# Kernel optimization log

Hardware: AMD Instinct MI355X
Metric: run time of the kernel (lower is better)

Reference implementation:

```python
import jax, jax.numpy as jnp
import numpy as np

HID = 6

def setup_inputs() -> dict:
    key = jax.random.key(0)
    k1, k2, k3, k4 = jax.random.split(key, 4)
    B, IN, OUT = 4194304, 20, 6
    x = jax.random.normal(k1, (B, IN), dtype=jnp.float32)
    # nn.Linear weights: shape [out_features, in_features], bias=False
    W1 = jax.random.normal(k2, (HID, IN), dtype=jnp.float32) / np.sqrt(IN)
    W2 = jax.random.normal(k3, (HID, HID), dtype=jnp.float32) / np.sqrt(HID)
    W5 = jax.random.normal(k4, (OUT, HID), dtype=jnp.float32) / np.sqrt(HID)
    return {"x": x, "W1": W1, "W2": W2, "W5": W5}

def reference(x, W1, W2, W5):
    # x = sigmoid(linear1(x)); x = sigmoid(linear2(x)); x = linear5(x)
    h = jax.nn.sigmoid(x @ W1.T)       # [B, 6]
    h = jax.nn.sigmoid(h @ W2.T)       # [B, 6]
    return h @ W5.T                    # [B, out]
```

## Files before the change

kernel.cpp:

```cpp
#include <hip/hip_runtime.h>

#define NIN  20
#define NHID 6
#define NOUT 6
#define RPB  256
#define PAD  21

__device__ __forceinline__ float fsig(float t) {
    return __builtin_amdgcn_rcpf(1.0f + __expf(-t));
}

__global__ __launch_bounds__(256, 4)
void mlp_fused(const float* __restrict__ x,
               const float* __restrict__ W1,
               const float* __restrict__ W2,
               const float* __restrict__ W5,
               float* __restrict__ out,
               int nrows)
{
    __shared__ float sx[RPB * PAD];

    const int t = threadIdx.x;
    const long long blk_row0 = (long long)blockIdx.x * RPB;
    const int rows_here = min(RPB, nrows - (int)min((long long)nrows, blk_row0));

    const float4* __restrict__ xp4 = (const float4*)(x + blk_row0 * NIN);
    const int n4 = rows_here * 5;
#pragma unroll
    for (int k = 0; k < 5; ++k) {
        const int i = t + RPB * k;
        if (i < n4) {
            float4 v = xp4[i];
            const int r = i / 5;
            const int c = 4 * (i % 5);
            float* d = &sx[r * PAD + c];
            d[0] = v.x; d[1] = v.y; d[2] = v.z; d[3] = v.w;
        }
    }
    __syncthreads();

    if (t >= rows_here) return;

    float xr[NIN];
#pragma unroll
    for (int k = 0; k < NIN; ++k) xr[k] = sx[t * PAD + k];

    float h[NHID];
#pragma unroll
    for (int j = 0; j < NHID; ++j) {
        float a = 0.0f;
#pragma unroll
        for (int k = 0; k < NIN; ++k) a = fmaf(xr[k], W1[j * NIN + k], a);
        h[j] = fsig(a);
    }

    float g[NHID];
#pragma unroll
    for (int j = 0; j < NHID; ++j) {
        float a = 0.0f;
#pragma unroll
        for (int k = 0; k < NHID; ++k) a = fmaf(h[k], W2[j * NHID + k], a);
        g[j] = fsig(a);
    }

    float o[NOUT];
#pragma unroll
    for (int j = 0; j < NOUT; ++j) {
        float a = 0.0f;
#pragma unroll
        for (int k = 0; k < NHID; ++k) a = fmaf(g[k], W5[j * NHID + k], a);
        o[j] = a;
    }

    float2* __restrict__ op = (float2*)(out + (blk_row0 + t) * NOUT);
    op[0] = make_float2(o[0], o[1]);
    op[1] = make_float2(o[2], o[3]);
    op[2] = make_float2(o[4], o[5]);
}

extern "C" void kernel_launch(void* const* d_in, const int* in_sizes, int n_in,
                              void* d_out, int out_size, void* d_ws, size_t ws_size,
                              hipStream_t stream) {
    const float* x  = (const float*)d_in[0];
    const float* W1 = (const float*)d_in[1];
    const float* W2 = (const float*)d_in[2];
    const float* W5 = (const float*)d_in[3];
    float* out = (float*)d_out;

    const int nrows = in_sizes[0] / NIN;
    const int grid  = (nrows + RPB - 1) / RPB;
    mlp_fused<<<grid, RPB, 0, stream>>>(x, W1, W2, W5, out, nrows);
}
```

Before: 469.4 us.

## Process four row chunks per block with register prefetch of next chunk

Each block now handles four 256-row chunks. While the current chunk is computed from shared memory, the next chunk's input is loaded into registers, so global loads overlap with compute and the grid shrinks fourfold. This adds an extra barrier per chunk and more register pressure, and with fewer blocks there is less parallelism available to hide memory latency on a bandwidth-bound kernel.

```diff
diff --git a/kernel.cpp b/kernel.cpp
--- a/kernel.cpp
+++ b/kernel.cpp
@@ -1,16 +1,17 @@
 #include <hip/hip_runtime.h>
 
-#define NIN  20
-#define NHID 6
-#define NOUT 6
-#define RPB  256
-#define PAD  21
+#define NIN    20
+#define NHID   6
+#define NOUT   6
+#define BS     256
+#define CHUNKS 4
+#define PAD    21
 
 __device__ __forceinline__ float fsig(float t) {
     return __builtin_amdgcn_rcpf(1.0f + __expf(-t));
 }
 
-__global__ __launch_bounds__(256, 4)
+__global__ __launch_bounds__(BS, 4)
 void mlp_fused(const float* __restrict__ x,
                const float* __restrict__ W1,
                const float* __restrict__ W2,
@@ -18,64 +19,88 @@
                float* __restrict__ out,
                int nrows)
 {
-    __shared__ float sx[RPB * PAD];
+    __shared__ float sx[BS * PAD];
 
     const int t = threadIdx.x;
-    const long long blk_row0 = (long long)blockIdx.x * RPB;
-    const int rows_here = min(RPB, nrows - (int)min((long long)nrows, blk_row0));
+    const long long block_row0 = (long long)blockIdx.x * (BS * CHUNKS);
 
-    const float4* __restrict__ xp4 = (const float4*)(x + blk_row0 * NIN);
-    const int n4 = rows_here * 5;
+    float4 pre[5];
+    {
+        const float4* __restrict__ p4 = (const float4*)(x + block_row0 * NIN);
+        const long long lim4 = ((long long)nrows - block_row0) * 5;
 #pragma unroll
-    for (int k = 0; k < 5; ++k) {
-        const int i = t + RPB * k;
-        if (i < n4) {
-            float4 v = xp4[i];
-            const int r = i / 5;
-            const int c = 4 * (i % 5);
-            float* d = &sx[r * PAD + c];
-            d[0] = v.x; d[1] = v.y; d[2] = v.z; d[3] = v.w;
+        for (int k = 0; k < 5; ++k) {
+            const int i = t + BS * k;
+            pre[k] = (i < lim4) ? p4[i] : make_float4(0.f, 0.f, 0.f, 0.f);
         }
     }
-    __syncthreads();
 
-    if (t >= rows_here) return;
+#pragma unroll
+    for (int c = 0; c < CHUNKS; ++c) {
+        const long long chunk_row0 = block_row0 + (long long)c * BS;
 
-    float xr[NIN];
 #pragma unroll
-    for (int k = 0; k < NIN; ++k) xr[k] = sx[t * PAD + k];
+        for (int k = 0; k < 5; ++k) {
+            const int i = t + BS * k;
+            const int r = i / 5;
+            const int q = (i % 5) * 4;
+            float* d = &sx[r * PAD + q];
+            d[0] = pre[k].x; d[1] = pre[k].y; d[2] = pre[k].z; d[3] = pre[k].w;
+        }
+        __syncthreads();
 
-    float h[NHID];
+        if (c + 1 < CHUNKS) {
+            const long long next_row0 = chunk_row0 + BS;
+            const float4* __restrict__ p4 = (const float4*)(x + next_row0 * NIN);
+            const long long lim4 = ((long long)nrows - next_row0) * 5;
 #pragma unroll
-    for (int j = 0; j < NHID; ++j) {
-        float a = 0.0f;
+            for (int k = 0; k < 5; ++k) {
+                const int i = t + BS * k;
+                pre[k] = (i < lim4) ? p4[i] : make_float4(0.f, 0.f, 0.f, 0.f);
+            }
+        }
+
+        const long long row = chunk_row0 + t;
+        if (row < nrows) {
+            float xr[NIN];
 #pragma unroll
-        for (int k = 0; k < NIN; ++k) a = fmaf(xr[k], W1[j * NIN + k], a);
-        h[j] = fsig(a);
+            for (int k = 0; k < NIN; ++k) xr[k] = sx[t * PAD + k];
+
+            float h[NHID];
+#pragma unroll
+            for (int j = 0; j < NHID; ++j) {
+                float a = 0.0f;
+#pragma unroll
+                for (int k = 0; k < NIN; ++k) a = fmaf(xr[k], W1[j * NIN + k], a);
+                h[j] = fsig(a);
+            }
+
+            float g[NHID];
+#pragma unroll
+            for (int j = 0; j < NHID; ++j) {
+                float a = 0.0f;
+#pragma unroll
+                for (int k = 0; k < NHID; ++k) a = fmaf(h[k], W2[j * NHID + k], a);
+                g[j] = fsig(a);
+            }
+
+            float o[NOUT];
+#pragma unroll
+            for (int j = 0; j < NOUT; ++j) {
+                float a = 0.0f;
+#pragma unroll
+                for (int k = 0; k < NHID; ++k) a = fmaf(g[k], W5[j * NHID + k], a);
+                o[j] = a;
+            }
+
+            float2* __restrict__ op = (float2*)(out + row * NOUT);
+            op[0] = make_float2(o[0], o[1]);
+            op[1] = make_float2(o[2], o[3]);
+            op[2] = make_float2(o[4], o[5]);
+        }
+
+        if (c + 1 < CHUNKS) __syncthreads();
     }
-
-    float g[NHID];
-#pragma unroll
-    for (int j = 0; j < NHID; ++j) {
-        float a = 0.0f;
-#pragma unroll
-        for (int k = 0; k < NHID; ++k) a = fmaf(h[k], W2[j * NHID + k], a);
-        g[j] = fsig(a);
-    }
-
-    float o[NOUT];
-#pragma unroll
-    for (int j = 0; j < NOUT; ++j) {
-        float a = 0.0f;
-#pragma unroll
-        for (int k = 0; k < NHID; ++k) a = fmaf(g[k], W5[j * NHID + k], a);
-        o[j] = a;
-    }
-
-    float2* __restrict__ op = (float2*)(out + (blk_row0 + t) * NOUT);
-    op[0] = make_float2(o[0], o[1]);
-    op[1] = make_float2(o[2], o[3]);
-    op[2] = make_float2(o[4], o[5]);
 }
 
 extern "C" void kernel_launch(void* const* d_in, const int* in_sizes, int n_in,
@@ -88,6 +113,7 @@
     float* out = (float*)d_out;
 
     const int nrows = in_sizes[0] / NIN;
-    const int grid  = (nrows + RPB - 1) / RPB;
-    mlp_fused<<<grid, RPB, 0, stream>>>(x, W1, W2, W5, out, nrows);
+    const int rows_per_block = BS * CHUNKS;
+    const int grid = (nrows + rows_per_block - 1) / rows_per_block;
+    mlp_fused<<<grid, BS, 0, stream>>>(x, W1, W2, W5, out, nrows);
 }
```

Result: no change. 470.1 us (+0.2%).
